# Performance work log

Hardware: AMD Instinct MI355X
Metric: run time of the kernel (lower is better)

## Reference

```python
import jax, jax.numpy as jnp
import numpy as np

B, S, E = 4, 2048, 512
H, D = 8, 64  # n_head, attn_dim


def setup_inputs() -> dict:
    key = jax.random.key(0)
    ks = jax.random.split(key, 12)
    scale = 0.02
    return {
        "input_q": jax.random.normal(ks[0], (B, S, E), dtype=jnp.float32),
        "input_k": jax.random.normal(ks[1], (B, S, E), dtype=jnp.float32),
        "input_v": jax.random.normal(ks[2], (B, S, E), dtype=jnp.float32),
        "mask": jax.random.randint(ks[3], (B, S, S), 0, 2, dtype=jnp.int32),
        "wq": jax.random.normal(ks[4], (E, H * D), dtype=jnp.float32) * scale,
        "bq": jnp.zeros((H * D,), dtype=jnp.float32),
        "wk": jax.random.normal(ks[5], (E, H * D), dtype=jnp.float32) * scale,
        "bk": jnp.zeros((H * D,), dtype=jnp.float32),
        "wv": jax.random.normal(ks[6], (E, H * D), dtype=jnp.float32) * scale,
        "bv": jnp.zeros((H * D,), dtype=jnp.float32),
        "wo": jax.random.normal(ks[7], (H * D, E), dtype=jnp.float32) * scale,
        "bo": jnp.zeros((E,), dtype=jnp.float32),
    }


def reference(input_q, input_k, input_v, mask, wq, bq, wk, bk, wv, bv, wo, bo):
    b, lq, _ = input_q.shape
    lk = input_k.shape[1]
    # projections -> [b, len, H, D] -> [b, H, len, D]
    q = (input_q @ wq + bq).reshape(b, lq, H, D).transpose(0, 2, 1, 3)
    k = (input_k @ wk + bk).reshape(b, lk, H, D).transpose(0, 2, 1, 3)
    v = (input_v @ wv + bv).reshape(b, lk, H, D).transpose(0, 2, 1, 3)
    # raw scores [b, H, lq, lk]
    score = jnp.einsum("bhqd,bhkd->bhqk", q, k)
    # NOTE: original masks with -1e9 BEFORE dividing by sqrt(attn_dim)
    score = jnp.where(mask[:, None, :, :] == 0, jnp.float32(-1e9), score)
    attn = jax.nn.softmax(score / jnp.sqrt(jnp.float32(D)), axis=-1)
    out = jnp.einsum("bhqk,bhkd->bqhd", attn, v).reshape(b, lq, H * D)
    return out @ wo + bo
```

## Files before the change

### kernel.cpp

```cpp
#include <hip/hip_runtime.h>
#include <hip/hip_bf16.h>
#include <stdint.h>

#define Bc 4
#define Sc 2048
#define Ec 512
#define Hc 8
#define Dc 64
#define HDc 512

typedef __attribute__((ext_vector_type(8))) short bf16x8;
typedef __attribute__((ext_vector_type(4))) float f32x4;
typedef unsigned int u32;

__device__ __forceinline__ unsigned short f2bf(float x) {
    union { float f; unsigned u; } v; v.f = x;
    unsigned r = v.u + 0x7FFFu + ((v.u >> 16) & 1u);
    return (unsigned short)(r >> 16);
}

__device__ __forceinline__ unsigned pkbf2(float a, float b) {
    float2 f; f.x = a; f.y = b;
    __hip_bfloat162 h = __float22bfloat162_rn(f);
    union { __hip_bfloat162 h2; unsigned u; } u; u.h2 = h;
    return u.u;
}

__device__ __forceinline__ uint4 pack8(float4 a, float4 b) {
    uint4 v;
    v.x = pkbf2(a.x, a.y); v.y = pkbf2(a.z, a.w);
    v.z = pkbf2(b.x, b.y); v.w = pkbf2(b.z, b.w);
    return v;
}

__device__ __forceinline__ void gload_lds(const void* g, void* l) {
    __builtin_amdgcn_global_load_lds(
        (const __attribute__((address_space(1))) u32*)g,
        (__attribute__((address_space(3))) u32*)l,
        16, 0, 0);
}

__global__ __launch_bounds__(256) void pack_mask(const int* __restrict__ mask,
                                                 unsigned long long* __restrict__ bits) {
    const int lane = threadIdx.x & 63;
    int wave = (blockIdx.x * blockDim.x + threadIdx.x) >> 6;
    const int nwaves = (gridDim.x * blockDim.x) >> 6;
    const int nwords = (Bc * Sc * Sc) / 64;
    for (int w = wave; w < nwords; w += nwaves) {
        int m = mask[(size_t)w * 64 + lane];
        unsigned long long b = __ballot(m != 0);
        if (lane == 0) bits[w] = b;
    }
}

__global__ __launch_bounds__(256) void transpose_w(
    const float* __restrict__ W0, const float* __restrict__ W1,
    const float* __restrict__ W2, const float* __restrict__ W3,
    unsigned short* __restrict__ Wt)
{
    const int z = blockIdx.z;
    const float* W = z == 0 ? W0 : (z == 1 ? W1 : (z == 2 ? W2 : W3));
    unsigned short* O = Wt + (size_t)z * Ec * HDc;
    __shared__ float t[64][65];
    const int k0 = blockIdx.x * 64, n0 = blockIdx.y * 64;
#pragma unroll
    for (int i = 0; i < 16; i++) {
        int idx = threadIdx.x + 256 * i;
        int kr = idx >> 6, nc = idx & 63;
        t[nc][kr] = W[(size_t)(k0 + kr) * HDc + n0 + nc];
    }
    __syncthreads();
#pragma unroll
    for (int i = 0; i < 16; i++) {
        int idx = threadIdx.x + 256 * i;
        int nr = idx >> 6, kc = idx & 63;
        O[(size_t)(n0 + nr) * Ec + k0 + kc] = f2bf(t[nr][kc]);
    }
}

template<int OMODE, bool ABF>
__global__ __launch_bounds__(256) void gemm_bt(
    const float* __restrict__ Af, const unsigned short* __restrict__ Ab,
    const unsigned short* __restrict__ Bt, const float* __restrict__ bias,
    unsigned short* __restrict__ Obf, float* __restrict__ Of)
{
    const int m0 = blockIdx.x * 128;
    const int n0 = blockIdx.y * 128;
    const int tid = threadIdx.x, lane = tid & 63, w = tid >> 6;
    const int c = lane & 15, quad = lane >> 4;
    const int wm = w & 1, wn = w >> 1;

    __shared__ unsigned short As[128 * 64];
    __shared__ unsigned short Bs[128 * 64];

    f32x4 acc[4][4];
#pragma unroll
    for (int i = 0; i < 4; i++)
#pragma unroll
        for (int j = 0; j < 4; j++) acc[i][j] = (f32x4){0.f, 0.f, 0.f, 0.f};

    for (int k0 = 0; k0 < Ec; k0 += 64) {
        __syncthreads();
#pragma unroll
        for (int jj = 0; jj < 4; jj++) {
            int rb = w * 32 + jj * 8;
            int row = rb + (lane >> 3);
            int dg = (lane & 7) ^ (row & 7);
            gload_lds(Bt + (size_t)(n0 + row) * Ec + k0 + dg * 8, &Bs[rb * 64]);
        }
        if (ABF) {
#pragma unroll
            for (int jj = 0; jj < 4; jj++) {
                int rb = w * 32 + jj * 8;
                int row = rb + (lane >> 3);
                int dg = (lane & 7) ^ (row & 7);
                gload_lds(Ab + (size_t)(m0 + row) * HDc + k0 + dg * 8, &As[rb * 64]);
            }
        } else {
#pragma unroll
            for (int s = 0; s < 4; s++) {
                int idx = tid + 256 * s;
                int row = idx >> 3, kp = idx & 7;
                int dg = kp ^ (row & 7);
                const float* src = Af + (size_t)(m0 + row) * Ec + k0 + dg * 8;
                float4 fa = *(const float4*)src;
                float4 fb = *(const float4*)(src + 4);
                *(uint4*)&As[row * 64 + kp * 8] = pack8(fa, fb);
            }
        }
        __syncthreads();
#pragma unroll
        for (int ks = 0; ks < 2; ks++) {
            int kg = ks * 4 + quad;
            bf16x8 af[4], bfr[4];
#pragma unroll
            for (int mt = 0; mt < 4; mt++) {
                int row = wm * 64 + mt * 16 + c;
                af[mt] = *(const bf16x8*)&As[row * 64 + ((kg ^ (row & 7)) * 8)];
            }
#pragma unroll
            for (int nt = 0; nt < 4; nt++) {
                int row = wn * 64 + nt * 16 + c;
                bfr[nt] = *(const bf16x8*)&Bs[row * 64 + ((kg ^ (row & 7)) * 8)];
            }
#pragma unroll
            for (int mt = 0; mt < 4; mt++)
#pragma unroll
                for (int nt = 0; nt < 4; nt++) {
                    if (OMODE == 1)
                        acc[mt][nt] = __builtin_amdgcn_mfma_f32_16x16x32_bf16(bfr[nt], af[mt], acc[mt][nt], 0, 0, 0);
                    else
                        acc[mt][nt] = __builtin_amdgcn_mfma_f32_16x16x32_bf16(af[mt], bfr[nt], acc[mt][nt], 0, 0, 0);
                }
        }
    }

    if (OMODE == 0) {
#pragma unroll
        for (int mt = 0; mt < 4; mt++)
#pragma unroll
            for (int r = 0; r < 4; r++) {
                int gm = m0 + wm * 64 + mt * 16 + quad * 4 + r;
#pragma unroll
                for (int nt = 0; nt < 4; nt++) {
                    int gn = n0 + wn * 64 + nt * 16 + c;
                    Obf[(size_t)gm * HDc + gn] = f2bf(acc[mt][nt][r] + bias[gn]);
                }
            }
    } else if (OMODE == 2) {
#pragma unroll
        for (int mt = 0; mt < 4; mt++)
#pragma unroll
            for (int r = 0; r < 4; r++) {
                int gm = m0 + wm * 64 + mt * 16 + quad * 4 + r;
#pragma unroll
                for (int nt = 0; nt < 4; nt++) {
                    int gn = n0 + wn * 64 + nt * 16 + c;
                    Of[(size_t)gm * Ec + gn] = acc[mt][nt][r] + bias[gn];
                }
            }
    } else {
        int tok = m0 + wm * 64 + 16 * 0 + c; (void)tok;
#pragma unroll
        for (int mt = 0; mt < 4; mt++) {
            int gm = m0 + wm * 64 + mt * 16 + c;
            int bb = gm >> 11, s = gm & (Sc - 1);
#pragma unroll
            for (int nt = 0; nt < 4; nt++)
#pragma unroll
                for (int r = 0; r < 4; r++) {
                    int ng = n0 + wn * 64 + nt * 16 + quad * 4 + r;
                    int h = ng >> 6, d = ng & 63;
                    Obf[((size_t)(bb * Hc + h) * Dc + d) * Sc + s] = f2bf(acc[mt][nt][r] + bias[ng]);
                }
        }
    }
}

__global__ __launch_bounds__(256) void attn_kernel(
    const unsigned short* __restrict__ Qb, const unsigned short* __restrict__ Kb,
    const unsigned short* __restrict__ Vt, const unsigned long long* __restrict__ Mb,
    unsigned short* __restrict__ Ob)
{
    const int qt = blockIdx.x;
    const int h  = blockIdx.y;
    const int b  = blockIdx.z;
    const int q0 = qt * 128;
    const int tid = threadIdx.x, lane = tid & 63, w = tid >> 6;
    const int c = lane & 15, quad = lane >> 4;

    __shared__ unsigned short Ks[2][64 * 64];
    __shared__ unsigned short Vs[2][64 * 64];
    __shared__ unsigned short Pt[128 * 64];

    const int q_g0 = q0 + w * 32 + c;
    const int q_g1 = q_g0 + 16;
    const size_t qoff0 = ((size_t)b * Sc + q_g0) * HDc + h * Dc;
    const size_t qoff1 = ((size_t)b * Sc + q_g1) * HDc + h * Dc;

    bf16x8 qf0[2], qf1[2];
#pragma unroll
    for (int ks = 0; ks < 2; ks++) {
        qf0[ks] = *(const bf16x8*)(Qb + qoff0 + ks * 32 + quad * 8);
        qf1[ks] = *(const bf16x8*)(Qb + qoff1 + ks * 32 + quad * 8);
    }

    const unsigned long long* mr0 = Mb + ((size_t)b * Sc + q_g0) * (Sc / 64);
    const unsigned long long* mr1 = Mb + ((size_t)b * Sc + q_g1) * (Sc / 64);
    const size_t kbase = ((size_t)b * Sc) * HDc + h * Dc;
    const size_t vbase = ((size_t)(b * Hc + h)) * Dc * Sc;

    f32x4 o0[4], o1[4];
#pragma unroll
    for (int i = 0; i < 4; i++) { o0[i] = (f32x4){0.f,0.f,0.f,0.f}; o1[i] = (f32x4){0.f,0.f,0.f,0.f}; }
    float ls0 = 0.f, ls1 = 0.f;

    unsigned short* pt0 = &Pt[(w * 32 + c) * 64];
    unsigned short* pt1 = pt0 + 16 * 64;
    const int sw = (c & 7) << 1;

    auto stage = [&](int kt, int buf) {
#pragma unroll
        for (int j = 0; j < 2; j++) {
            int rb = w * 16 + j * 8;
            int row = rb + (lane >> 3);
            int dg = (lane & 7) ^ (row & 7);
            gload_lds(Kb + kbase + (size_t)(kt * 64 + row) * HDc + dg * 8, &Ks[buf][rb * 64]);
            gload_lds(Vt + vbase + (size_t)row * Sc + kt * 64 + dg * 8, &Vs[buf][rb * 64]);
        }
    };

    stage(0, 0);
    for (int kt = 0; kt < Sc / 64; kt++) {
        const int cur = kt & 1;
        unsigned long long mw0 = mr0[kt];
        unsigned long long mw1 = mr1[kt];
        __syncthreads();
        if (kt + 1 < Sc / 64) stage(kt + 1, cur ^ 1);

        f32x4 s0[4], s1[4];
#pragma unroll
        for (int nt = 0; nt < 4; nt++) { s0[nt] = (f32x4){0.f,0.f,0.f,0.f}; s1[nt] = (f32x4){0.f,0.f,0.f,0.f}; }
#pragma unroll
        for (int ks = 0; ks < 2; ks++) {
            int kg = ks * 4 + quad;
#pragma unroll
            for (int nt = 0; nt < 4; nt++) {
                int t = nt * 16 + c;
                bf16x8 a = *(const bf16x8*)&Ks[cur][t * 64 + ((kg ^ (t & 7)) * 8)];
                s0[nt] = __builtin_amdgcn_mfma_f32_16x16x32_bf16(a, qf0[ks], s0[nt], 0, 0, 0);
                s1[nt] = __builtin_amdgcn_mfma_f32_16x16x32_bf16(a, qf1[ks], s1[nt], 0, 0, 0);
            }
        }

#pragma unroll
        for (int nt = 0; nt < 4; nt++) {
            float p0[4], p1[4];
#pragma unroll
            for (int r = 0; r < 4; r++) {
                int sh = nt * 16 + quad * 4 + r;
                float e0 = __expf(s0[nt][r] * 0.125f);
                float e1 = __expf(s1[nt][r] * 0.125f);
                p0[r] = ((mw0 >> sh) & 1ull) ? e0 : 0.f;
                p1[r] = ((mw1 >> sh) & 1ull) ? e1 : 0.f;
                ls0 += p0[r]; ls1 += p1[r];
            }
            int u = nt * 4 + quad;
            uint2 k0v, k1v;
            k0v.x = pkbf2(p0[0], p0[1]); k0v.y = pkbf2(p0[2], p0[3]);
            k1v.x = pkbf2(p1[0], p1[1]); k1v.y = pkbf2(p1[2], p1[3]);
            *(uint2*)(pt0 + ((u ^ sw) << 2)) = k0v;
            *(uint2*)(pt1 + ((u ^ sw) << 2)) = k1v;
        }

#pragma unroll
        for (int ks = 0; ks < 2; ks++) {
            int u1 = ks * 8 + quad * 2;
            bf16x8 pf0 = *(const bf16x8*)(pt0 + ((u1 ^ sw) << 2));
            bf16x8 pf1 = *(const bf16x8*)(pt1 + ((u1 ^ sw) << 2));
            int kg = ks * 4 + quad;
#pragma unroll
            for (int nt = 0; nt < 4; nt++) {
                int d = nt * 16 + c;
                bf16x8 a = *(const bf16x8*)&Vs[cur][d * 64 + ((kg ^ (d & 7)) * 8)];
                o0[nt] = __builtin_amdgcn_mfma_f32_16x16x32_bf16(a, pf0, o0[nt], 0, 0, 0);
                o1[nt] = __builtin_amdgcn_mfma_f32_16x16x32_bf16(a, pf1, o1[nt], 0, 0, 0);
            }
        }
    }

    ls0 += __shfl_xor(ls0, 16, 64); ls0 += __shfl_xor(ls0, 32, 64);
    ls1 += __shfl_xor(ls1, 16, 64); ls1 += __shfl_xor(ls1, 32, 64);
    float inv0 = 1.0f / ls0, inv1 = 1.0f / ls1;

#pragma unroll
    for (int nt = 0; nt < 4; nt++) {
        uint2 a, bpk;
        a.x = pkbf2(o0[nt][0] * inv0, o0[nt][1] * inv0);
        a.y = pkbf2(o0[nt][2] * inv0, o0[nt][3] * inv0);
        bpk.x = pkbf2(o1[nt][0] * inv1, o1[nt][1] * inv1);
        bpk.y = pkbf2(o1[nt][2] * inv1, o1[nt][3] * inv1);
        *(uint2*)(Ob + qoff0 + nt * 16 + quad * 4) = a;
        *(uint2*)(Ob + qoff1 + nt * 16 + quad * 4) = bpk;
    }
}

extern "C" void kernel_launch(void* const* d_in, const int* in_sizes, int n_in,
                              void* d_out, int out_size, void* d_ws, size_t ws_size,
                              hipStream_t stream)
{
    const float* xq = (const float*)d_in[0];
    const float* xk = (const float*)d_in[1];
    const float* xv = (const float*)d_in[2];
    const int* mask = (const int*)d_in[3];
    const float* wq = (const float*)d_in[4];
    const float* bq = (const float*)d_in[5];
    const float* wk = (const float*)d_in[6];
    const float* bk = (const float*)d_in[7];
    const float* wv = (const float*)d_in[8];
    const float* bv = (const float*)d_in[9];
    const float* wo = (const float*)d_in[10];
    const float* bo = (const float*)d_in[11];
    float* out = (float*)d_out;

    char* ws = (char*)d_ws;
    unsigned short* qb = (unsigned short*)(ws + (size_t)0 * 1024 * 1024);
    unsigned short* kb = (unsigned short*)(ws + (size_t)8 * 1024 * 1024);
    unsigned short* vt = (unsigned short*)(ws + (size_t)16 * 1024 * 1024);
    unsigned short* ab = (unsigned short*)(ws + (size_t)24 * 1024 * 1024);
    unsigned long long* mb = (unsigned long long*)(ws + (size_t)32 * 1024 * 1024);
    unsigned short* wt = (unsigned short*)(ws + (size_t)48 * 1024 * 1024);

    hipLaunchKernelGGL(pack_mask, dim3(2048), dim3(256), 0, stream, mask, mb);
    hipLaunchKernelGGL(transpose_w, dim3(8, 8, 4), dim3(256), 0, stream,
                       wq, wk, wv, wo, wt);

    const size_t WSZ = (size_t)Ec * HDc;
    hipLaunchKernelGGL((gemm_bt<0, false>), dim3(64, 4), dim3(256), 0, stream,
                       xq, (const unsigned short*)nullptr, wt + 0 * WSZ, bq, qb, (float*)nullptr);
    hipLaunchKernelGGL((gemm_bt<0, false>), dim3(64, 4), dim3(256), 0, stream,
                       xk, (const unsigned short*)nullptr, wt + 1 * WSZ, bk, kb, (float*)nullptr);
    hipLaunchKernelGGL((gemm_bt<1, false>), dim3(64, 4), dim3(256), 0, stream,
                       xv, (const unsigned short*)nullptr, wt + 2 * WSZ, bv, vt, (float*)nullptr);

    hipLaunchKernelGGL(attn_kernel, dim3(16, 8, 4), dim3(256), 0, stream,
                       qb, kb, vt, mb, ab);

    hipLaunchKernelGGL((gemm_bt<2, true>), dim3(64, 4), dim3(256), 0, stream,
                       (const float*)nullptr, ab, wt + 3 * WSZ, bo, (unsigned short*)nullptr, out);
}
```

Measured before the change: 306.2 us.

## Merge QKV projections into one launch, halve attention query tile, retile output GEMM

Merges the three projection GEMMs into one launch with a z-dimension that selects Q, K or V, and swaps grid axes so N-tiles of the same M-tile run adjacently. The attention kernel now processes 64 queries per block instead of 128, doubling the grid to 1024 blocks with launch bounds for 4 blocks per CU. Masking is folded into the exponent as a large negative bias, with the scale folded into exp2. A dedicated output GEMM uses 64-row M tiles, giving 512 blocks. The aim is better CU occupancy and less launch overhead, at the cost of more K/V reloads per query and more staging work per block.

After: 301.7 us. About the same (-1.5%).

```diff
diff --git a/kernel.cpp b/kernel.cpp
--- a/kernel.cpp
+++ b/kernel.cpp
@@ -78,14 +78,20 @@
     }
 }
 
-template<int OMODE, bool ABF>
-__global__ __launch_bounds__(256) void gemm_bt(
-    const float* __restrict__ Af, const unsigned short* __restrict__ Ab,
-    const unsigned short* __restrict__ Bt, const float* __restrict__ bias,
-    unsigned short* __restrict__ Obf, float* __restrict__ Of)
+__global__ __launch_bounds__(256) void proj_gemm(
+    const float* __restrict__ Xq, const float* __restrict__ Xk, const float* __restrict__ Xv,
+    const unsigned short* __restrict__ Wt,
+    const float* __restrict__ bq, const float* __restrict__ bk, const float* __restrict__ bv,
+    unsigned short* __restrict__ Oq, unsigned short* __restrict__ Ok,
+    unsigned short* __restrict__ Vt)
 {
-    const int m0 = blockIdx.x * 128;
-    const int n0 = blockIdx.y * 128;
+    const int z = blockIdx.z;
+    const float* X = z == 0 ? Xq : (z == 1 ? Xk : Xv);
+    const unsigned short* Bt = Wt + (size_t)z * Ec * HDc;
+    const float* bias = z == 0 ? bq : (z == 1 ? bk : bv);
+
+    const int n0 = blockIdx.x * 128;
+    const int m0 = blockIdx.y * 128;
     const int tid = threadIdx.x, lane = tid & 63, w = tid >> 6;
     const int c = lane & 15, quad = lane >> 4;
     const int wm = w & 1, wn = w >> 1;
@@ -108,25 +114,15 @@
             int dg = (lane & 7) ^ (row & 7);
             gload_lds(Bt + (size_t)(n0 + row) * Ec + k0 + dg * 8, &Bs[rb * 64]);
         }
-        if (ABF) {
-#pragma unroll
-            for (int jj = 0; jj < 4; jj++) {
-                int rb = w * 32 + jj * 8;
-                int row = rb + (lane >> 3);
-                int dg = (lane & 7) ^ (row & 7);
-                gload_lds(Ab + (size_t)(m0 + row) * HDc + k0 + dg * 8, &As[rb * 64]);
-            }
-        } else {
-#pragma unroll
-            for (int s = 0; s < 4; s++) {
-                int idx = tid + 256 * s;
-                int row = idx >> 3, kp = idx & 7;
-                int dg = kp ^ (row & 7);
-                const float* src = Af + (size_t)(m0 + row) * Ec + k0 + dg * 8;
-                float4 fa = *(const float4*)src;
-                float4 fb = *(const float4*)(src + 4);
-                *(uint4*)&As[row * 64 + kp * 8] = pack8(fa, fb);
-            }
+#pragma unroll
+        for (int s = 0; s < 4; s++) {
+            int idx = tid + 256 * s;
+            int row = idx >> 3, kp = idx & 7;
+            int dg = kp ^ (row & 7);
+            const float* src = X + (size_t)(m0 + row) * Ec + k0 + dg * 8;
+            float4 fa = *(const float4*)src;
+            float4 fb = *(const float4*)(src + 4);
+            *(uint4*)&As[row * 64 + kp * 8] = pack8(fa, fb);
         }
         __syncthreads();
 #pragma unroll
@@ -143,19 +139,24 @@
                 int row = wn * 64 + nt * 16 + c;
                 bfr[nt] = *(const bf16x8*)&Bs[row * 64 + ((kg ^ (row & 7)) * 8)];
             }
-#pragma unroll
-            for (int mt = 0; mt < 4; mt++)
-#pragma unroll
-                for (int nt = 0; nt < 4; nt++) {
-                    if (OMODE == 1)
+            if (z < 2) {
+#pragma unroll
+                for (int mt = 0; mt < 4; mt++)
+#pragma unroll
+                    for (int nt = 0; nt < 4; nt++)
+                        acc[mt][nt] = __builtin_amdgcn_mfma_f32_16x16x32_bf16(af[mt], bfr[nt], acc[mt][nt], 0, 0, 0);
+            } else {
+#pragma unroll
+                for (int mt = 0; mt < 4; mt++)
+#pragma unroll
+                    for (int nt = 0; nt < 4; nt++)
                         acc[mt][nt] = __builtin_amdgcn_mfma_f32_16x16x32_bf16(bfr[nt], af[mt], acc[mt][nt], 0, 0, 0);
-                    else
-                        acc[mt][nt] = __builtin_amdgcn_mfma_f32_16x16x32_bf16(af[mt], bfr[nt], acc[mt][nt], 0, 0, 0);
-                }
-        }
-    }
-
-    if (OMODE == 0) {
+            }
+        }
+    }
+
+    if (z < 2) {
+        unsigned short* O = z == 0 ? Oq : Ok;
 #pragma unroll
         for (int mt = 0; mt < 4; mt++)
 #pragma unroll
@@ -164,40 +165,27 @@
 #pragma unroll
                 for (int nt = 0; nt < 4; nt++) {
                     int gn = n0 + wn * 64 + nt * 16 + c;
-                    Obf[(size_t)gm * HDc + gn] = f2bf(acc[mt][nt][r] + bias[gn]);
+                    O[(size_t)gm * HDc + gn] = f2bf(acc[mt][nt][r] + bias[gn]);
                 }
             }
-    } else if (OMODE == 2) {
-#pragma unroll
-        for (int mt = 0; mt < 4; mt++)
-#pragma unroll
-            for (int r = 0; r < 4; r++) {
-                int gm = m0 + wm * 64 + mt * 16 + quad * 4 + r;
-#pragma unroll
-                for (int nt = 0; nt < 4; nt++) {
-                    int gn = n0 + wn * 64 + nt * 16 + c;
-                    Of[(size_t)gm * Ec + gn] = acc[mt][nt][r] + bias[gn];
-                }
-            }
     } else {
-        int tok = m0 + wm * 64 + 16 * 0 + c; (void)tok;
 #pragma unroll
         for (int mt = 0; mt < 4; mt++) {
             int gm = m0 + wm * 64 + mt * 16 + c;
-            int bb = gm >> 11, s = gm & (Sc - 1);
+            int bb = gm >> 11, sPos = gm & (Sc - 1);
 #pragma unroll
             for (int nt = 0; nt < 4; nt++)
 #pragma unroll
                 for (int r = 0; r < 4; r++) {
                     int ng = n0 + wn * 64 + nt * 16 + quad * 4 + r;
-                    int h = ng >> 6, d = ng & 63;
-                    Obf[((size_t)(bb * Hc + h) * Dc + d) * Sc + s] = f2bf(acc[mt][nt][r] + bias[ng]);
+                    int hh = ng >> 6, d = ng & 63;
+                    Vt[((size_t)(bb * Hc + hh) * Dc + d) * Sc + sPos] = f2bf(acc[mt][nt][r] + bias[ng]);
                 }
         }
     }
 }
 
-__global__ __launch_bounds__(256) void attn_kernel(
+__global__ __launch_bounds__(256, 4) void attn_kernel(
     const unsigned short* __restrict__ Qb, const unsigned short* __restrict__ Kb,
     const unsigned short* __restrict__ Vt, const unsigned long long* __restrict__ Mb,
     unsigned short* __restrict__ Ob)
@@ -205,38 +193,31 @@
     const int qt = blockIdx.x;
     const int h  = blockIdx.y;
     const int b  = blockIdx.z;
-    const int q0 = qt * 128;
+    const int q0 = qt * 64;
     const int tid = threadIdx.x, lane = tid & 63, w = tid >> 6;
     const int c = lane & 15, quad = lane >> 4;
 
     __shared__ unsigned short Ks[2][64 * 64];
     __shared__ unsigned short Vs[2][64 * 64];
-    __shared__ unsigned short Pt[128 * 64];
-
-    const int q_g0 = q0 + w * 32 + c;
-    const int q_g1 = q_g0 + 16;
-    const size_t qoff0 = ((size_t)b * Sc + q_g0) * HDc + h * Dc;
-    const size_t qoff1 = ((size_t)b * Sc + q_g1) * HDc + h * Dc;
-
-    bf16x8 qf0[2], qf1[2];
-#pragma unroll
-    for (int ks = 0; ks < 2; ks++) {
-        qf0[ks] = *(const bf16x8*)(Qb + qoff0 + ks * 32 + quad * 8);
-        qf1[ks] = *(const bf16x8*)(Qb + qoff1 + ks * 32 + quad * 8);
-    }
-
-    const unsigned long long* mr0 = Mb + ((size_t)b * Sc + q_g0) * (Sc / 64);
-    const unsigned long long* mr1 = Mb + ((size_t)b * Sc + q_g1) * (Sc / 64);
+    __shared__ unsigned short Pt[64 * 64];
+
+    const int qg = q0 + w * 16 + c;
+    const size_t qoff = ((size_t)b * Sc + qg) * HDc + h * Dc;
+
+    bf16x8 qf[2];
+    qf[0] = *(const bf16x8*)(Qb + qoff + quad * 8);
+    qf[1] = *(const bf16x8*)(Qb + qoff + 32 + quad * 8);
+
+    const unsigned long long* mr = Mb + ((size_t)b * Sc + qg) * (Sc / 64);
     const size_t kbase = ((size_t)b * Sc) * HDc + h * Dc;
     const size_t vbase = ((size_t)(b * Hc + h)) * Dc * Sc;
 
-    f32x4 o0[4], o1[4];
-#pragma unroll
-    for (int i = 0; i < 4; i++) { o0[i] = (f32x4){0.f,0.f,0.f,0.f}; o1[i] = (f32x4){0.f,0.f,0.f,0.f}; }
-    float ls0 = 0.f, ls1 = 0.f;
-
-    unsigned short* pt0 = &Pt[(w * 32 + c) * 64];
-    unsigned short* pt1 = pt0 + 16 * 64;
+    f32x4 o[4];
+#pragma unroll
+    for (int i = 0; i < 4; i++) o[i] = (f32x4){0.f, 0.f, 0.f, 0.f};
+    float lsum = 0.f;
+
+    unsigned short* ptrow = &Pt[(w * 16 + c) * 64];
     const int sw = (c & 7) << 1;
 
     auto stage = [&](int kt, int buf) {
@@ -253,14 +234,13 @@
     stage(0, 0);
     for (int kt = 0; kt < Sc / 64; kt++) {
         const int cur = kt & 1;
-        unsigned long long mw0 = mr0[kt];
-        unsigned long long mw1 = mr1[kt];
+        unsigned long long mw = mr[kt];
         __syncthreads();
         if (kt + 1 < Sc / 64) stage(kt + 1, cur ^ 1);
 
-        f32x4 s0[4], s1[4];
-#pragma unroll
-        for (int nt = 0; nt < 4; nt++) { s0[nt] = (f32x4){0.f,0.f,0.f,0.f}; s1[nt] = (f32x4){0.f,0.f,0.f,0.f}; }
+        f32x4 s[4];
+#pragma unroll
+        for (int nt = 0; nt < 4; nt++) s[nt] = (f32x4){0.f, 0.f, 0.f, 0.f};
 #pragma unroll
         for (int ks = 0; ks < 2; ks++) {
             int kg = ks * 4 + quad;
@@ -268,61 +248,124 @@
             for (int nt = 0; nt < 4; nt++) {
                 int t = nt * 16 + c;
                 bf16x8 a = *(const bf16x8*)&Ks[cur][t * 64 + ((kg ^ (t & 7)) * 8)];
-                s0[nt] = __builtin_amdgcn_mfma_f32_16x16x32_bf16(a, qf0[ks], s0[nt], 0, 0, 0);
-                s1[nt] = __builtin_amdgcn_mfma_f32_16x16x32_bf16(a, qf1[ks], s1[nt], 0, 0, 0);
-            }
-        }
-
+                s[nt] = __builtin_amdgcn_mfma_f32_16x16x32_bf16(a, qf[ks], s[nt], 0, 0, 0);
+            }
+        }
+
+        u32 nlo = ~(u32)(mw >> (quad * 4));
+        u32 nhi = ~(u32)(mw >> (quad * 4 + 32));
 #pragma unroll
         for (int nt = 0; nt < 4; nt++) {
-            float p0[4], p1[4];
+            u32 msrc = (nt < 2) ? nlo : nhi;
+            float p[4];
 #pragma unroll
             for (int r = 0; r < 4; r++) {
-                int sh = nt * 16 + quad * 4 + r;
-                float e0 = __expf(s0[nt][r] * 0.125f);
-                float e1 = __expf(s1[nt][r] * 0.125f);
-                p0[r] = ((mw0 >> sh) & 1ull) ? e0 : 0.f;
-                p1[r] = ((mw1 >> sh) & 1ull) ? e1 : 0.f;
-                ls0 += p0[r]; ls1 += p1[r];
-            }
+                const int sh = (nt & 1) * 16 + r;
+                int tneg = ((int)(msrc << (31 - sh))) >> 31;
+                float bias = __int_as_float(tneg & 0xC4800000);
+                p[r] = exp2f(fmaf(s[nt][r], 0.18033688f, bias));
+                lsum += p[r];
+            }
+            uint2 pk; pk.x = pkbf2(p[0], p[1]); pk.y = pkbf2(p[2], p[3]);
             int u = nt * 4 + quad;
-            uint2 k0v, k1v;
-            k0v.x = pkbf2(p0[0], p0[1]); k0v.y = pkbf2(p0[2], p0[3]);
-            k1v.x = pkbf2(p1[0], p1[1]); k1v.y = pkbf2(p1[2], p1[3]);
-            *(uint2*)(pt0 + ((u ^ sw) << 2)) = k0v;
-            *(uint2*)(pt1 + ((u ^ sw) << 2)) = k1v;
+            *(uint2*)(ptrow + ((u ^ sw) << 2)) = pk;
         }
 
 #pragma unroll
         for (int ks = 0; ks < 2; ks++) {
             int u1 = ks * 8 + quad * 2;
-            bf16x8 pf0 = *(const bf16x8*)(pt0 + ((u1 ^ sw) << 2));
-            bf16x8 pf1 = *(const bf16x8*)(pt1 + ((u1 ^ sw) << 2));
+            bf16x8 pf = *(const bf16x8*)(ptrow + ((u1 ^ sw) << 2));
             int kg = ks * 4 + quad;
 #pragma unroll
             for (int nt = 0; nt < 4; nt++) {
                 int d = nt * 16 + c;
                 bf16x8 a = *(const bf16x8*)&Vs[cur][d * 64 + ((kg ^ (d & 7)) * 8)];
-                o0[nt] = __builtin_amdgcn_mfma_f32_16x16x32_bf16(a, pf0, o0[nt], 0, 0, 0);
-                o1[nt] = __builtin_amdgcn_mfma_f32_16x16x32_bf16(a, pf1, o1[nt], 0, 0, 0);
-            }
-        }
-    }
-
-    ls0 += __shfl_xor(ls0, 16, 64); ls0 += __shfl_xor(ls0, 32, 64);
-    ls1 += __shfl_xor(ls1, 16, 64); ls1 += __shfl_xor(ls1, 32, 64);
-    float inv0 = 1.0f / ls0, inv1 = 1.0f / ls1;
+                o[nt] = __builtin_amdgcn_mfma_f32_16x16x32_bf16(a, pf, o[nt], 0, 0, 0);
+            }
+        }
+    }
+
+    lsum += __shfl_xor(lsum, 16, 64);
+    lsum += __shfl_xor(lsum, 32, 64);
+    float inv = 1.0f / lsum;
 
 #pragma unroll
     for (int nt = 0; nt < 4; nt++) {
-        uint2 a, bpk;
-        a.x = pkbf2(o0[nt][0] * inv0, o0[nt][1] * inv0);
-        a.y = pkbf2(o0[nt][2] * inv0, o0[nt][3] * inv0);
-        bpk.x = pkbf2(o1[nt][0] * inv1, o1[nt][1] * inv1);
-        bpk.y = pkbf2(o1[nt][2] * inv1, o1[nt][3] * inv1);
-        *(uint2*)(Ob + qoff0 + nt * 16 + quad * 4) = a;
-        *(uint2*)(Ob + qoff1 + nt * 16 + quad * 4) = bpk;
-    }
+        uint2 pk;
+        pk.x = pkbf2(o[nt][0] * inv, o[nt][1] * inv);
+        pk.y = pkbf2(o[nt][2] * inv, o[nt][3] * inv);
+        *(uint2*)(Ob + qoff + nt * 16 + quad * 4) = pk;
+    }
+}
+
+__global__ __launch_bounds__(256) void out_gemm(
+    const unsigned short* __restrict__ Ab, const unsigned short* __restrict__ Bt,
+    const float* __restrict__ bias, float* __restrict__ Out)
+{
+    const int n0 = blockIdx.x * 128;
+    const int m0 = blockIdx.y * 64;
+    const int tid = threadIdx.x, lane = tid & 63, w = tid >> 6;
+    const int c = lane & 15, quad = lane >> 4;
+    const int wm = w & 1, wn = w >> 1;
+
+    __shared__ unsigned short As[64 * 64];
+    __shared__ unsigned short Bs[128 * 64];
+
+    f32x4 acc[2][4];
+#pragma unroll
+    for (int i = 0; i < 2; i++)
+#pragma unroll
+        for (int j = 0; j < 4; j++) acc[i][j] = (f32x4){0.f, 0.f, 0.f, 0.f};
+
+    for (int k0 = 0; k0 < HDc; k0 += 64) {
+        __syncthreads();
+#pragma unroll
+        for (int jj = 0; jj < 4; jj++) {
+            int rb = w * 32 + jj * 8;
+            int row = rb + (lane >> 3);
+            int dg = (lane & 7) ^ (row & 7);
+            gload_lds(Bt + (size_t)(n0 + row) * Ec + k0 + dg * 8, &Bs[rb * 64]);
+        }
+#pragma unroll
+        for (int jj = 0; jj < 2; jj++) {
+            int rb = w * 16 + jj * 8;
+            int row = rb + (lane >> 3);
+            int dg = (lane & 7) ^ (row & 7);
+            gload_lds(Ab + (size_t)(m0 + row) * HDc + k0 + dg * 8, &As[rb * 64]);
+        }
+        __syncthreads();
+#pragma unroll
+        for (int ks = 0; ks < 2; ks++) {
+            int kg = ks * 4 + quad;
+            bf16x8 af[2], bfr[4];
+#pragma unroll
+            for (int mt = 0; mt < 2; mt++) {
+                int row = wm * 32 + mt * 16 + c;
+                af[mt] = *(const bf16x8*)&As[row * 64 + ((kg ^ (row & 7)) * 8)];
+            }
+#pragma unroll
+            for (int nt = 0; nt < 4; nt++) {
+                int row = wn * 64 + nt * 16 + c;
+                bfr[nt] = *(const bf16x8*)&Bs[row * 64 + ((kg ^ (row & 7)) * 8)];
+            }
+#pragma unroll
+            for (int mt = 0; mt < 2; mt++)
+#pragma unroll
+                for (int nt = 0; nt < 4; nt++)
+                    acc[mt][nt] = __builtin_amdgcn_mfma_f32_16x16x32_bf16(af[mt], bfr[nt], acc[mt][nt], 0, 0, 0);
+        }
+    }
+#pragma unroll
+    for (int mt = 0; mt < 2; mt++)
+#pragma unroll
+        for (int r = 0; r < 4; r++) {
+            int gm = m0 + wm * 32 + mt * 16 + quad * 4 + r;
+#pragma unroll
+            for (int nt = 0; nt < 4; nt++) {
+                int gn = n0 + wn * 64 + nt * 16 + c;
+                Out[(size_t)gm * Ec + gn] = acc[mt][nt][r] + bias[gn];
+            }
+        }
 }
 
 extern "C" void kernel_launch(void* const* d_in, const int* in_sizes, int n_in,
@@ -356,16 +399,12 @@
                        wq, wk, wv, wo, wt);
 
     const size_t WSZ = (size_t)Ec * HDc;
-    hipLaunchKernelGGL((gemm_bt<0, false>), dim3(64, 4), dim3(256), 0, stream,
-                       xq, (const unsigned short*)nullptr, wt + 0 * WSZ, bq, qb, (float*)nullptr);
-    hipLaunchKernelGGL((gemm_bt<0, false>), dim3(64, 4), dim3(256), 0, stream,
-                       xk, (const unsigned short*)nullptr, wt + 1 * WSZ, bk, kb, (float*)nullptr);
-    hipLaunchKernelGGL((gemm_bt<1, false>), dim3(64, 4), dim3(256), 0, stream,
-                       xv, (const unsigned short*)nullptr, wt + 2 * WSZ, bv, vt, (float*)nullptr);
-
-    hipLaunchKernelGGL(attn_kernel, dim3(16, 8, 4), dim3(256), 0, stream,
+    hipLaunchKernelGGL(proj_gemm, dim3(4, 64, 3), dim3(256), 0, stream,
+                       xq, xk, xv, wt, bq, bk, bv, qb, kb, vt);
+
+    hipLaunchKernelGGL(attn_kernel, dim3(32, 8, 4), dim3(256), 0, stream,
                        qb, kb, vt, mb, ab);
 
-    hipLaunchKernelGGL((gemm_bt<2, true>), dim3(64, 4), dim3(256), 0, stream,
-                       (const float*)nullptr, ab, wt + 3 * WSZ, bo, (unsigned short*)nullptr, out);
-}
+    hipLaunchKernelGGL(out_gemm, dim3(4, 128), dim3(256), 0, stream,
+                       ab, wt + 3 * WSZ, bo, out);
+}
```
